# Kernel tuning notes

Hardware: AMD Instinct MI355X
Metric: run time of the kernel (lower is better)

The kernel has to match this reference:

```python
import jax, jax.numpy as jnp
import numpy as np

DIM = 1536; NH = 12; HD = 128; C2 = HD // 2          # rope half-dim = 64
F, H, W = 1, 30, 52
FRAME = H * W                                         # 1560 tokens/frame
SINK_FRAMES = 1; LOCAL_ATTN = 6
SINK = SINK_FRAMES * FRAME                            # 1560
MAX_ATTN = LOCAL_ATTN * 1560                          # 9360
CACHE = 9360                                          # kv cache length
GLOBAL_END = 9360; LOCAL_END_CACHE = 9360             # cache state before step
SPLITS = (C2 - 2 * (C2 // 3), C2 // 3, C2 // 3)       # (22, 21, 21)
EPS = 1e-6


def setup_inputs() -> dict:
    key = jax.random.key(0)
    ks = jax.random.split(key, 12)
    s = F * H * W
    rn = lambda k, sh, sc=1.0: jax.random.normal(k, sh, jnp.float32) * sc
    x = rn(ks[0], (1, s, DIM))
    Wq = rn(ks[1], (DIM, DIM), 0.02); Wk = rn(ks[2], (DIM, DIM), 0.02)
    Wv = rn(ks[3], (DIM, DIM), 0.02); Wo = rn(ks[4], (DIM, DIM), 0.02)
    zb = jnp.zeros((DIM,), jnp.float32)
    angles = jax.random.uniform(ks[5], (1024, C2), jnp.float32) * (2.0 * np.pi)
    freqs_cos = jnp.cos(angles); freqs_sin = jnp.sin(angles)
    cache_k = rn(ks[6], (1, CACHE, NH, HD)); cache_v = rn(ks[7], (1, CACHE, NH, HD))
    return dict(x=x, Wq=Wq, bq=zb, Wk=Wk, bk=zb, Wv=Wv, bv=zb, Wo=Wo, bo=zb,
                nq_w=jnp.ones((DIM,), jnp.float32), nk_w=jnp.ones((DIM,), jnp.float32),
                cache_k=cache_k, cache_v=cache_v,
                freqs_cos=freqs_cos, freqs_sin=freqs_sin,
                seq_lens=jnp.array([s], jnp.int32),
                grid_sizes=jnp.array([[F, H, W]], jnp.int32),
                current_start=GLOBAL_END)


def _rmsnorm(x, w):
    return x * jax.lax.rsqrt(jnp.mean(x * x, -1, keepdims=True) + EPS) * w


def _grid_table(table, start_frame):
    """table [1024, C2] -> per-token rope factors [S, 1, C2] over the (F,H,W) grid."""
    s0, s1, s2 = SPLITS
    tf, th, tw = table[:, :s0], table[:, s0:s0 + s1], table[:, s0 + s1:]
    fp = jnp.broadcast_to(tf[start_frame:start_frame + F][:, None, None, :], (F, H, W, s0))
    hp = jnp.broadcast_to(th[:H][None, :, None, :], (F, H, W, s1))
    wp = jnp.broadcast_to(tw[:W][None, None, :, :], (F, H, W, s2))
    return jnp.concatenate([fp, hp, wp], -1).reshape(F * H * W, 1, C2)


def _rope(x, cos, sin):
    # x: [b, s, n, d]; cos/sin: [s, 1, C2] (complex multiply in real arithmetic)
    b, s, n, d = x.shape
    xp = x.reshape(b, s, n, d // 2, 2)
    xr, xi = xp[..., 0], xp[..., 1]
    c, sn = cos[None], sin[None]                      # [1, s, 1, C2]
    out_r = xr * c - xi * sn
    out_i = xr * sn + xi * c
    return jnp.stack([out_r, out_i], -1).reshape(b, s, n, d)


def reference(x, Wq, bq, Wk, bk, Wv, bv, Wo, bo, nq_w, nk_w,
              cache_k, cache_v, freqs_cos, freqs_sin,
              seq_lens, grid_sizes, current_start):
    b, s = x.shape[:2]
    q = _rmsnorm(x @ Wq.T + bq, nq_w).reshape(b, s, NH, HD)
    k = _rmsnorm(x @ Wk.T + bk, nk_w).reshape(b, s, NH, HD)
    v = (x @ Wv.T + bv).reshape(b, s, NH, HD)

    start_frame = int(current_start) // FRAME
    cos = _grid_table(freqs_cos, start_frame)
    sin = _grid_table(freqs_sin, start_frame)
    rq = _rope(q, cos, sin)
    rk = _rope(k, cos, sin)

    # --- static cache bookkeeping (roll_and_insert path; all Python ints) ---
    num_new = s
    current_end = int(current_start) + num_new
    num_evicted = num_new + LOCAL_END_CACHE - CACHE           # 1560
    num_rolled = LOCAL_END_CACHE - num_evicted - SINK         # 6240
    local_end = LOCAL_END_CACHE + current_end - GLOBAL_END - num_evicted  # 9360
    local_start = local_end - num_new                         # 7800 == SINK + num_rolled
    temp_k = jnp.concatenate(
        [cache_k[:, :SINK], cache_k[:, SINK + num_evicted:SINK + num_evicted + num_rolled], rk], axis=1)
    temp_v = jnp.concatenate(
        [cache_v[:, :SINK], cache_v[:, SINK + num_evicted:SINK + num_evicted + num_rolled], v], axis=1)

    # --- sink + sliding-window attention ---
    local_budget = MAX_ATTN - SINK
    win_start = max(SINK, local_end - local_budget)
    k_cat = jnp.concatenate([temp_k[:, :SINK], temp_k[:, win_start:local_end]], axis=1)
    v_cat = jnp.concatenate([temp_v[:, :SINK], temp_v[:, win_start:local_end]], axis=1)

    logits = jnp.einsum('bqhd,bkhd->bhqk', rq, k_cat) * (HD ** -0.5)
    probs = jax.nn.softmax(logits, axis=-1)
    out = jnp.einsum('bhqk,bkhd->bqhd', probs, v_cat)
    y = out.reshape(b, s, DIM) @ Wo.T + bo
    return y
```

## Files before the change

kernel.cpp:

```cpp
#include <hip/hip_runtime.h>
#include <hip/hip_bf16.h>

typedef __bf16 bf16;
typedef __bf16 bf16x2 __attribute__((ext_vector_type(2)));
typedef __bf16 bf16x4 __attribute__((ext_vector_type(4)));
typedef __bf16 bf16x8 __attribute__((ext_vector_type(8)));
typedef float f32x4 __attribute__((ext_vector_type(4)));
typedef float f32x16 __attribute__((ext_vector_type(16)));

#define DIM 1536
#define NH 12
#define HD 128
#define SEQ 1560
#define KV 9360
#define KVP 9408
#define SINK 1560
#define NEWBASE 7800
#define QSCALE_L2E (0.08838834764831845f * 1.4426950408889634f)
#define NSPLIT 3
#define CHUNK 3136
#define NT 49
#define QBLK 128
#define NQT 13

__device__ __forceinline__ void gl_lds16(const void* g, void* l) {
  __builtin_amdgcn_global_load_lds(
      (const __attribute__((address_space(1))) unsigned int*)g,
      (__attribute__((address_space(3))) unsigned int*)l, 16, 0, 0);
}

__device__ __forceinline__ f32x16 mfma32(bf16x8 a, bf16x8 b, f32x16 c) {
  return __builtin_amdgcn_mfma_f32_32x32x16_bf16(a, b, c, 0, 0, 0);
}

struct CastBatch {
  const float* src[5];
  bf16* dst[5];
  int n[5];
};
__global__ __launch_bounds__(256) void castall(CastBatch cb) {
  const float* src = cb.src[blockIdx.y];
  bf16* dst = cb.dst[blockIdx.y];
  int n = cb.n[blockIdx.y];
  int i = (blockIdx.x * 256 + threadIdx.x) * 8;
  if (i < n) {
    float4 a = *(const float4*)(src + i);
    float4 b = *(const float4*)(src + i + 4);
    bf16x8 o;
    o[0] = (bf16)a.x; o[1] = (bf16)a.y; o[2] = (bf16)a.z; o[3] = (bf16)a.w;
    o[4] = (bf16)b.x; o[5] = (bf16)b.y; o[6] = (bf16)b.z; o[7] = (bf16)b.w;
    *(bf16x8*)(dst + i) = o;
  }
}

__global__ __launch_bounds__(256) void clear_pad(bf16* __restrict__ Kcat,
                                                 bf16* __restrict__ Vt) {
  int h = blockIdx.y;
  int i = blockIdx.x * 256 + threadIdx.x;
  if (i < (KVP - KV) * HD) {
    int r = KV + i / HD, d = i % HD;
    Kcat[((size_t)h * KVP + r) * HD + d] = (bf16)0.f;
    int dv = i / (KVP - KV), j = KV + i % (KVP - KV);
    Vt[((size_t)h * HD + dv) * KVP + j] = (bf16)0.f;
  }
}

struct GemmBatch {
  const bf16* B[3];
  const float* bias[3];
  float* C[3];
};

#define BM 128
#define BN 128
#define BK 32

__global__ __launch_bounds__(256, 2) void gemm_bt(const bf16* __restrict__ A,
                                                  GemmBatch gb, int M) {
  const bf16* Bw = gb.B[blockIdx.z];
  const float* bias = gb.bias[blockIdx.z];
  float* C = gb.C[blockIdx.z];
  int bm = blockIdx.x * BM;
  int bn = blockIdx.y * BN;

  __shared__ bf16 Alds[2][BM][BK];
  __shared__ bf16 Blds[2][BN][BK];

  int t = threadIdx.x;
  int lane = t & 63;
  int wave = t >> 6;
  int wr = wave >> 1, wc = wave & 1;
  int fr = lane & 15;
  int fo = (lane >> 4) * 8;

  f32x4 acc[4][4] = {};

  const int NK = DIM / BK;
  int colA = (lane & 3) * 8;
  int lrow = lane >> 2;

#define STAGEG(buf, k0)                                                     \
  {                                                                         \
    _Pragma("unroll") for (int p = 0; p < 2; ++p) {                         \
      int rbase = wave * 16 + p * 64;                                       \
      int ga = bm + rbase + lrow;                                           \
      if (ga > M - 1) ga = M - 1;                                           \
      gl_lds16(A + (size_t)ga * DIM + (k0) + colA, &Alds[buf][rbase][0]);   \
      int gbv = bn + rbase + lrow;                                          \
      gl_lds16(Bw + (size_t)gbv * DIM + (k0) + colA, &Blds[buf][rbase][0]); \
    }                                                                       \
  }

  STAGEG(0, 0);
  int cur = 0;
  for (int ks = 0; ks < NK; ++ks) {
    __syncthreads();
    if (ks + 1 < NK) STAGEG(cur ^ 1, (ks + 1) * BK);
    bf16x8 af[4], bfv[4];
#pragma unroll
    for (int i = 0; i < 4; ++i)
      af[i] = *(const bf16x8*)&Alds[cur][wr * 64 + i * 16 + fr][fo];
#pragma unroll
    for (int j = 0; j < 4; ++j)
      bfv[j] = *(const bf16x8*)&Blds[cur][wc * 64 + j * 16 + fr][fo];
#pragma unroll
    for (int i = 0; i < 4; ++i)
#pragma unroll
      for (int j = 0; j < 4; ++j)
        acc[i][j] = __builtin_amdgcn_mfma_f32_16x16x32_bf16(af[i], bfv[j],
                                                            acc[i][j], 0, 0, 0);
    cur ^= 1;
  }
#undef STAGEG

  int g4 = (lane >> 4) * 4;
#pragma unroll
  for (int i = 0; i < 4; ++i) {
    int mbase = bm + wr * 64 + i * 16 + g4;
#pragma unroll
    for (int j = 0; j < 4; ++j) {
      int col = bn + wc * 64 + j * 16 + fr;
      float bv = bias[col];
#pragma unroll
      for (int r = 0; r < 4; ++r) {
        int m = mbase + r;
        if (m < M) C[(size_t)m * DIM + col] = acc[i][j][r] + bv;
      }
    }
  }
}

__global__ __launch_bounds__(256) void norm_rope(
    const float* __restrict__ qraw, const float* __restrict__ kraw,
    const float* __restrict__ nqw, const float* __restrict__ nkw,
    const float* __restrict__ fcos, const float* __restrict__ fsin,
    bf16* __restrict__ Qh, bf16* __restrict__ Kcat) {
  int tok = blockIdx.x;
  int tid = threadIdx.x;
  const float* qr = qraw + (size_t)tok * DIM;
  const float* kr = kraw + (size_t)tok * DIM;
  float sq = 0.f, sk = 0.f;
  for (int c = tid; c < DIM; c += 256) {
    float a = qr[c];
    sq += a * a;
    float b = kr[c];
    sk += b * b;
  }
#pragma unroll
  for (int off = 32; off; off >>= 1) {
    sq += __shfl_down(sq, off);
    sk += __shfl_down(sk, off);
  }
  __shared__ float red[2][4];
  int w = tid >> 6;
  if ((tid & 63) == 0) {
    red[0][w] = sq;
    red[1][w] = sk;
  }
  __syncthreads();
  sq = red[0][0] + red[0][1] + red[0][2] + red[0][3];
  sk = red[1][0] + red[1][1] + red[1][2] + red[1][3];
  float rsq = rsqrtf(sq * (1.0f / DIM) + 1e-6f);
  float rsk = rsqrtf(sk * (1.0f / DIM) + 1e-6f);

  int hrow = tok / 52, wrow = tok % 52;
  for (int p = tid; p < NH * 64; p += 256) {
    int n = p >> 6, i = p & 63;
    int trow = (i < 22) ? 6 : (i < 43 ? hrow : wrow);
    float cs = fcos[trow * 64 + i];
    float sn = fsin[trow * 64 + i];
    int c = n * HD + 2 * i;
    float xr = qr[c] * rsq * nqw[c];
    float xi = qr[c + 1] * rsq * nqw[c + 1];
    bf16x2 qo;
    qo[0] = (bf16)((xr * cs - xi * sn) * QSCALE_L2E);
    qo[1] = (bf16)((xr * sn + xi * cs) * QSCALE_L2E);
    *(bf16x2*)(Qh + ((size_t)n * SEQ + tok) * HD + 2 * i) = qo;
    float yr = kr[c] * rsk * nkw[c];
    float yi = kr[c + 1] * rsk * nkw[c + 1];
    bf16x2 ko;
    ko[0] = (bf16)(yr * cs - yi * sn);
    ko[1] = (bf16)(yr * sn + yi * cs);
    *(bf16x2*)(Kcat + ((size_t)n * KVP + NEWBASE + tok) * HD + 2 * i) = ko;
  }
}

__global__ __launch_bounds__(256) void build_kcat(const float* __restrict__ cache_k,
                                                  bf16* __restrict__ Kcat) {
  int j = blockIdx.x;
  int src = j < SINK ? j : j + SINK;
  const float* sp = cache_k + (size_t)src * DIM;
  for (int c4 = threadIdx.x; c4 < DIM / 4; c4 += 256) {
    float4 v = *(const float4*)(sp + c4 * 4);
    int c = c4 * 4;
    int n = c >> 7, d = c & 127;
    bf16x4 o;
    o[0] = (bf16)v.x; o[1] = (bf16)v.y; o[2] = (bf16)v.z; o[3] = (bf16)v.w;
    *(bf16x4*)(Kcat + ((size_t)n * KVP + j) * HD + d) = o;
  }
}

__global__ __launch_bounds__(256) void build_vt(const float* __restrict__ cache_v,
                                                const float* __restrict__ vraw,
                                                bf16* __restrict__ Vt) {
  int h = blockIdx.y;
  int j0 = blockIdx.x * 64;
  __shared__ bf16 T[128][72];
  int tid = threadIdx.x;
  for (int idx = tid; idx < 64 * 32; idx += 256) {
    int jl = idx >> 5, s = idx & 31;
    int j = j0 + jl;
    if (j >= KV) continue;
    const float* sp;
    if (j < NEWBASE) {
      int srcj = j < SINK ? j : j + SINK;
      sp = cache_v + (size_t)srcj * DIM + h * HD;
    } else {
      sp = vraw + (size_t)(j - NEWBASE) * DIM + h * HD;
    }
    float4 v = *(const float4*)(sp + s * 4);
    T[s * 4 + 0][jl] = (bf16)v.x;
    T[s * 4 + 1][jl] = (bf16)v.y;
    T[s * 4 + 2][jl] = (bf16)v.z;
    T[s * 4 + 3][jl] = (bf16)v.w;
  }
  __syncthreads();
  for (int idx = tid; idx < 128 * 16; idx += 256) {
    int d = idx >> 4, g = idx & 15;
    int j = j0 + g * 4;
    if (j + 4 > KV) continue;
    bf16x4 o;
    o[0] = T[d][4 * g];
    o[1] = T[d][4 * g + 1];
    o[2] = T[d][4 * g + 2];
    o[3] = T[d][4 * g + 3];
    *(bf16x4*)(Vt + ((size_t)h * HD + d) * KVP + j) = o;
  }
}

__global__ __launch_bounds__(256, 2) void attn_split(const bf16* __restrict__ Qh,
                                                     const bf16* __restrict__ Kcat,
                                                     const bf16* __restrict__ Vtg,
                                                     float* __restrict__ Opart,
                                                     float* __restrict__ MLpart) {
  int orig = blockIdx.x;
  int xcd = orig & 7, jj = orig >> 3;
  int wgid = (xcd < 4 ? xcd * 59 : 236 + (xcd - 4) * 58) + jj;
  int qt = wgid % NQT;
  int h = (wgid / NQT) % NH;
  int sp = wgid / (NQT * NH);
  int q0 = qt * QBLK;
  int c0 = sp * CHUNK;

  int t = threadIdx.x, lane = t & 63, w = t >> 6;
  int ql = lane & 31, hi = lane >> 5;

  __shared__ __align__(16) bf16 Klds[2][64 * 128];
  __shared__ __align__(16) bf16 Vlds[2][128 * 64];

  int qrow = q0 + w * 32 + ql;
  int qcl = qrow < SEQ ? qrow : SEQ - 1;
  const bf16* Qp = Qh + ((size_t)h * SEQ + qcl) * HD + hi * 8;
  bf16x8 qreg[8];
#pragma unroll
  for (int ks = 0; ks < 8; ++ks) qreg[ks] = *(const bf16x8*)(Qp + ks * 16);

  int kadd[4], vadd[4];
#pragma unroll
  for (int p = 0; p < 4; ++p) {
    int rK = (4 * w + p) * 4 + (lane >> 4);
    int cK = (lane & 15) ^ (rK & 15);
    kadd[p] = rK * HD + cK * 8;
    int dV = (4 * w + p) * 8 + (lane >> 3);
    int cV = (lane & 7) ^ (dV & 7);
    vadd[p] = dV * KVP + cV * 8;
  }

  int koff[2][8];
#pragma unroll
  for (int kb = 0; kb < 2; ++kb)
#pragma unroll
    for (int ks = 0; ks < 8; ++ks)
      koff[kb][ks] = (kb * 32 + ql) * 256 + (((ks * 2 + hi) ^ (ql & 15)) * 16);
  int voff[4][4];
#pragma unroll
  for (int db = 0; db < 4; ++db)
#pragma unroll
    for (int ks = 0; ks < 4; ++ks)
      voff[db][ks] = (db * 32 + ql) * 128 + (((ks * 2 + hi) ^ (ql & 7)) * 16);

  const bf16* Khp = Kcat + (size_t)h * KVP * HD;
  const bf16* Vhp = Vtg + (size_t)h * HD * KVP;

  f32x16 oacc[4] = {};
  float m_q = -1e38f, l_q = 0.f;

#define STAGE(buf, j0)                                                        \
  {                                                                           \
    const bf16* Ks = Khp + (size_t)(j0)*HD;                                   \
    const bf16* Vs = Vhp + (j0);                                              \
    _Pragma("unroll") for (int p = 0; p < 4; ++p) {                           \
      gl_lds16(Ks + kadd[p], (char*)&Klds[buf][0] + w * 4096 + p * 1024);     \
      gl_lds16(Vs + vadd[p], (char*)&Vlds[buf][0] + w * 4096 + p * 1024);     \
    }                                                                         \
  }

  STAGE(0, c0);
  __syncthreads();
  int cur = 0;

  for (int ti = 0; ti < NT; ++ti) {
    int j0 = c0 + ti * 64;
    if (ti + 1 < NT) STAGE(cur ^ 1, j0 + 64);

    const char* Kc = (const char*)&Klds[cur][0];
    const char* Vc = (const char*)&Vlds[cur][0];

    f32x16 s0 = {}, s1 = {};
    __builtin_amdgcn_s_setprio(1);
#pragma unroll
    for (int ks = 0; ks < 8; ++ks) {
      s0 = mfma32(*(const bf16x8*)(Kc + koff[0][ks]), qreg[ks], s0);
      s1 = mfma32(*(const bf16x8*)(Kc + koff[1][ks]), qreg[ks], s1);
    }
    __builtin_amdgcn_s_setprio(0);

    if (j0 + 64 > KV) {
#pragma unroll
      for (int reg = 0; reg < 16; ++reg) {
        int kk = (reg & 3) + 8 * (reg >> 2) + 4 * hi;
        if (j0 + kk >= KV) s0[reg] = -1e38f;
        if (j0 + 32 + kk >= KV) s1[reg] = -1e38f;
      }
    }

    f32x16 mm;
#pragma unroll
    for (int r = 0; r < 16; ++r) mm[r] = fmaxf(s0[r], s1[r]);
    float m8[8];
#pragma unroll
    for (int r = 0; r < 8; ++r) m8[r] = fmaxf(mm[r], mm[r + 8]);
    float mx = fmaxf(fmaxf(fmaxf(m8[0], m8[4]), fmaxf(m8[1], m8[5])),
                     fmaxf(fmaxf(m8[2], m8[6]), fmaxf(m8[3], m8[7])));
    mx = fmaxf(mx, __shfl_xor(mx, 32));

    if (__any(mx - m_q > 8.f)) {
      float mnew = fmaxf(m_q, mx);
      float corr = exp2f(m_q - mnew);
      m_q = mnew;
      l_q *= corr;
#pragma unroll
      for (int reg = 0; reg < 16; ++reg) {
        int qsrc = (reg & 3) + 8 * (reg >> 2) + 4 * hi;
        float c = __shfl(corr, qsrc);
#pragma unroll
        for (int db = 0; db < 4; ++db) oacc[db][reg] *= c;
      }
    }

#pragma unroll
    for (int r = 0; r < 16; ++r) {
      s0[r] = exp2f(s0[r] - m_q);
      s1[r] = exp2f(s1[r] - m_q);
    }
    f32x16 ss;
#pragma unroll
    for (int r = 0; r < 16; ++r) ss[r] = s0[r] + s1[r];
    float t8[8];
#pragma unroll
    for (int r = 0; r < 8; ++r) t8[r] = ss[r] + ss[r + 8];
    float sum = ((t8[0] + t8[4]) + (t8[1] + t8[5])) +
                ((t8[2] + t8[6]) + (t8[3] + t8[7]));
    sum += __shfl_xor(sum, 32);
    l_q += sum;

    bf16x8 pa[4];
#pragma unroll
    for (int ks = 0; ks < 4; ++ks) {
      const f32x16& S = (ks < 2) ? s0 : s1;
      const int r0 = (ks & 1) * 8;
      bf16x2 p0, p1, p2, p3;
      p0[0] = (bf16)S[r0 + 0]; p0[1] = (bf16)S[r0 + 1];
      p1[0] = (bf16)S[r0 + 2]; p1[1] = (bf16)S[r0 + 3];
      p2[0] = (bf16)S[r0 + 4]; p2[1] = (bf16)S[r0 + 5];
      p3[0] = (bf16)S[r0 + 6]; p3[1] = (bf16)S[r0 + 7];
      int x0 = __builtin_bit_cast(int, p0);
      int x1 = __builtin_bit_cast(int, p1);
      int y0 = __builtin_bit_cast(int, p2);
      int y1 = __builtin_bit_cast(int, p3);
      int sx0 = __shfl_xor(x0, 32);
      int sx1 = __shfl_xor(x1, 32);
      int sy0 = __shfl_xor(y0, 32);
      int sy1 = __shfl_xor(y1, 32);
      int4 tmp;
      tmp.x = hi ? sy0 : x0;
      tmp.y = hi ? sy1 : x1;
      tmp.z = hi ? y0 : sx0;
      tmp.w = hi ? y1 : sx1;
      pa[ks] = __builtin_bit_cast(bf16x8, tmp);
    }

    __builtin_amdgcn_s_setprio(1);
#pragma unroll
    for (int db = 0; db < 4; ++db)
#pragma unroll
      for (int ks = 0; ks < 4; ++ks)
        oacc[db] = mfma32(pa[ks], *(const bf16x8*)(Vc + voff[db][ks]), oacc[db]);
    __builtin_amdgcn_s_setprio(0);

    __syncthreads();
    cur ^= 1;
  }
#undef STAGE

  float* Oh = Opart + ((size_t)sp * NH + h) * SEQ * HD;
  float* MLh = MLpart + ((size_t)sp * NH + h) * SEQ * 2;
#pragma unroll
  for (int reg = 0; reg < 16; ++reg) {
    int q = q0 + w * 32 + (reg & 3) + 8 * (reg >> 2) + 4 * hi;
    if (q >= SEQ) continue;
#pragma unroll
    for (int db = 0; db < 4; ++db)
      Oh[(size_t)q * HD + db * 32 + ql] = oacc[db][reg];
  }
  if (lane < 32) {
    int q = q0 + w * 32 + ql;
    if (q < SEQ) {
      MLh[q * 2 + 0] = m_q;
      MLh[q * 2 + 1] = l_q;
    }
  }
}

__global__ __launch_bounds__(256) void attn_merge(const float* __restrict__ Opart,
                                                  const float* __restrict__ MLpart,
                                                  bf16* __restrict__ Aout) {
  int idx = blockIdx.x * 2 + (threadIdx.x >> 7);
  if (idx >= NH * SEQ) return;
  int d = threadIdx.x & 127;
  int h = idx / SEQ, q = idx % SEQ;
  float m[NSPLIT];
  float M = -1e38f;
#pragma unroll
  for (int s = 0; s < NSPLIT; ++s) {
    m[s] = MLpart[(((size_t)s * NH + h) * SEQ + q) * 2];
    M = fmaxf(M, m[s]);
  }
  float L = 0.f, o = 0.f;
#pragma unroll
  for (int s = 0; s < NSPLIT; ++s) {
    float wgt = exp2f(m[s] - M);
    L += MLpart[(((size_t)s * NH + h) * SEQ + q) * 2 + 1] * wgt;
    o += Opart[((((size_t)s * NH + h) * SEQ + q)) * HD + d] * wgt;
  }
  Aout[(size_t)q * DIM + h * HD + d] = (bf16)(o / L);
}

extern "C" void kernel_launch(void* const* d_in, const int* in_sizes, int n_in,
                              void* d_out, int out_size, void* d_ws, size_t ws_size,
                              hipStream_t stream) {
  const float* x = (const float*)d_in[0];
  const float* Wq = (const float*)d_in[1];
  const float* bq = (const float*)d_in[2];
  const float* Wk = (const float*)d_in[3];
  const float* bk = (const float*)d_in[4];
  const float* Wv = (const float*)d_in[5];
  const float* bv = (const float*)d_in[6];
  const float* Wo = (const float*)d_in[7];
  const float* bo = (const float*)d_in[8];
  const float* nqw = (const float*)d_in[9];
  const float* nkw = (const float*)d_in[10];
  const float* cache_k = (const float*)d_in[11];
  const float* cache_v = (const float*)d_in[12];
  const float* fcos = (const float*)d_in[13];
  const float* fsin = (const float*)d_in[14];
  float* out = (float*)d_out;

  char* ws = (char*)d_ws;
  size_t off = 0;
  auto alloc = [&](size_t bytes) {
    char* p = ws + off;
    off += (bytes + 255) & ~(size_t)255;
    return p;
  };
  const int XN = SEQ * DIM;
  const int WN = DIM * DIM;
  bf16* xb = (bf16*)alloc((size_t)XN * 2);
  bf16* Wqb = (bf16*)alloc((size_t)WN * 2);
  bf16* Wkb = (bf16*)alloc((size_t)WN * 2);
  bf16* Wvb = (bf16*)alloc((size_t)WN * 2);
  bf16* Wob = (bf16*)alloc((size_t)WN * 2);
  bf16* QhB = (bf16*)alloc((size_t)NH * SEQ * HD * 2);
  bf16* Kcat = (bf16*)alloc((size_t)NH * KVP * HD * 2);
  bf16* Vt = (bf16*)alloc((size_t)NH * HD * KVP * 2);
  bf16* Aout = (bf16*)alloc((size_t)XN * 2);
  float* MLpart = (float*)alloc((size_t)NSPLIT * NH * SEQ * 2 * 4);
  float* Opart = (float*)alloc((size_t)NSPLIT * NH * SEQ * HD * 4);
  float* qraw = Opart;
  float* kraw = qraw + XN;
  float* vraw = kraw + XN;

  CastBatch cb;
  cb.src[0] = x;  cb.dst[0] = xb;  cb.n[0] = XN;
  cb.src[1] = Wq; cb.dst[1] = Wqb; cb.n[1] = WN;
  cb.src[2] = Wk; cb.dst[2] = Wkb; cb.n[2] = WN;
  cb.src[3] = Wv; cb.dst[3] = Wvb; cb.n[3] = WN;
  cb.src[4] = Wo; cb.dst[4] = Wob; cb.n[4] = WN;
  castall<<<dim3((XN + 2047) / 2048, 5), 256, 0, stream>>>(cb);

  clear_pad<<<dim3(((KVP - KV) * HD + 255) / 256, NH), 256, 0, stream>>>(Kcat, Vt);

  GemmBatch gqkv;
  gqkv.B[0] = Wqb; gqkv.B[1] = Wkb; gqkv.B[2] = Wvb;
  gqkv.bias[0] = bq; gqkv.bias[1] = bk; gqkv.bias[2] = bv;
  gqkv.C[0] = qraw; gqkv.C[1] = kraw; gqkv.C[2] = vraw;
  gemm_bt<<<dim3(13, 12, 3), 256, 0, stream>>>(xb, gqkv, SEQ);

  norm_rope<<<SEQ, 256, 0, stream>>>(qraw, kraw, nqw, nkw, fcos, fsin, QhB, Kcat);
  build_kcat<<<NEWBASE, 256, 0, stream>>>(cache_k, Kcat);
  build_vt<<<dim3(147, NH), 256, 0, stream>>>(cache_v, vraw, Vt);

  attn_split<<<dim3(NQT * NH * NSPLIT), 256, 0, stream>>>(QhB, Kcat, Vt, Opart, MLpart);
  attn_merge<<<(NH * SEQ + 1) / 2, 256, 0, stream>>>(Opart, MLpart, Aout);

  GemmBatch gout;
  gout.B[0] = Wob; gout.B[1] = Wob; gout.B[2] = Wob;
  gout.bias[0] = bo; gout.bias[1] = bo; gout.bias[2] = bo;
  gout.C[0] = out; gout.C[1] = out; gout.C[2] = out;
  gemm_bt<<<dim3(13, 12, 1), 256, 0, stream>>>(Aout, gout, SEQ);
}
```

Baseline: 310.4 us.

## Halve KV tile to 32, double split count, raise occupancy, use permlane32_swap

The attention kernel now processes 32 keys per tile instead of 64 and splits the KV range into 6 chunks instead of 3. This doubles the number of workgroups and halves LDS and register use, and launch bounds now ask for 4 waves per SIMD to hide latency better. The P-matrix lane exchange uses permlane32_swap in place of four shuffles plus selects. In exchange there are twice as many loop iterations with syncs, less MFMA work per barrier, and more partial outputs for the combine step to merge. The host launch grid and combine kernel must match the new split count, and that code is not visible here.

```diff
diff --git a/kernel.cpp b/kernel.cpp
--- a/kernel.cpp
+++ b/kernel.cpp
@@ -7,6 +7,7 @@
 typedef __bf16 bf16x8 __attribute__((ext_vector_type(8)));
 typedef float f32x4 __attribute__((ext_vector_type(4)));
 typedef float f32x16 __attribute__((ext_vector_type(16)));
+typedef unsigned u32x2 __attribute__((ext_vector_type(2)));
 
 #define DIM 1536
 #define NH 12
@@ -17,9 +18,10 @@
 #define SINK 1560
 #define NEWBASE 7800
 #define QSCALE_L2E (0.08838834764831845f * 1.4426950408889634f)
-#define NSPLIT 3
-#define CHUNK 3136
+#define NSPLIT 6
+#define CHUNK 1568
 #define NT 49
+#define KB 32
 #define QBLK 128
 #define NQT 13
 
@@ -258,25 +260,25 @@
   }
 }
 
-__global__ __launch_bounds__(256, 2) void attn_split(const bf16* __restrict__ Qh,
+__global__ __launch_bounds__(256, 4) void attn_split(const bf16* __restrict__ Qh,
                                                      const bf16* __restrict__ Kcat,
                                                      const bf16* __restrict__ Vtg,
                                                      float* __restrict__ Opart,
                                                      float* __restrict__ MLpart) {
   int orig = blockIdx.x;
-  int xcd = orig & 7, jj = orig >> 3;
-  int wgid = (xcd < 4 ? xcd * 59 : 236 + (xcd - 4) * 58) + jj;
+  int wgid = (orig & 7) * 117 + (orig >> 3);
   int qt = wgid % NQT;
-  int h = (wgid / NQT) % NH;
-  int sp = wgid / (NQT * NH);
+  int rest = wgid / NQT;
+  int h = rest % NH;
+  int sp = rest / NH;
   int q0 = qt * QBLK;
   int c0 = sp * CHUNK;
 
   int t = threadIdx.x, lane = t & 63, w = t >> 6;
   int ql = lane & 31, hi = lane >> 5;
 
-  __shared__ __align__(16) bf16 Klds[2][64 * 128];
-  __shared__ __align__(16) bf16 Vlds[2][128 * 64];
+  __shared__ __align__(16) bf16 Klds[2][KB * 128];
+  __shared__ __align__(16) bf16 Vlds[2][128 * KB];
 
   int qrow = q0 + w * 32 + ql;
   int qcl = qrow < SEQ ? qrow : SEQ - 1;
@@ -285,29 +287,26 @@
 #pragma unroll
   for (int ks = 0; ks < 8; ++ks) qreg[ks] = *(const bf16x8*)(Qp + ks * 16);
 
-  int kadd[4], vadd[4];
-#pragma unroll
-  for (int p = 0; p < 4; ++p) {
-    int rK = (4 * w + p) * 4 + (lane >> 4);
-    int cK = (lane & 15) ^ (rK & 15);
-    kadd[p] = rK * HD + cK * 8;
-    int dV = (4 * w + p) * 8 + (lane >> 3);
-    int cV = (lane & 7) ^ (dV & 7);
-    vadd[p] = dV * KVP + cV * 8;
-  }
-
-  int koff[2][8];
-#pragma unroll
-  for (int kb = 0; kb < 2; ++kb)
-#pragma unroll
-    for (int ks = 0; ks < 8; ++ks)
-      koff[kb][ks] = (kb * 32 + ql) * 256 + (((ks * 2 + hi) ^ (ql & 15)) * 16);
-  int voff[4][4];
+  int kadd[2], vadd[2];
+#pragma unroll
+  for (int p = 0; p < 2; ++p) {
+    int m = (2 * w + p) * 64 + lane;
+    int rK = m >> 4, cK = m & 15;
+    kadd[p] = rK * HD + (cK ^ (rK & 15)) * 8;
+    int dV = m >> 2, cV = m & 3;
+    vadd[p] = dV * KVP + (cV ^ (dV & 3)) * 8;
+  }
+
+  int koff[8];
+#pragma unroll
+  for (int ks = 0; ks < 8; ++ks)
+    koff[ks] = ql * 256 + (((ks * 2 + hi) ^ (ql & 15)) * 16);
+  int voff[4][2];
 #pragma unroll
   for (int db = 0; db < 4; ++db)
 #pragma unroll
-    for (int ks = 0; ks < 4; ++ks)
-      voff[db][ks] = (db * 32 + ql) * 128 + (((ks * 2 + hi) ^ (ql & 7)) * 16);
+    for (int ks = 0; ks < 2; ++ks)
+      voff[db][ks] = (db * 32 + ql) * 64 + (((ks * 2 + hi) ^ (ql & 3)) * 16);
 
   const bf16* Khp = Kcat + (size_t)h * KVP * HD;
   const bf16* Vhp = Vtg + (size_t)h * HD * KVP;
@@ -319,9 +318,9 @@
   {                                                                           \
     const bf16* Ks = Khp + (size_t)(j0)*HD;                                   \
     const bf16* Vs = Vhp + (j0);                                              \
-    _Pragma("unroll") for (int p = 0; p < 4; ++p) {                           \
-      gl_lds16(Ks + kadd[p], (char*)&Klds[buf][0] + w * 4096 + p * 1024);     \
-      gl_lds16(Vs + vadd[p], (char*)&Vlds[buf][0] + w * 4096 + p * 1024);     \
+    _Pragma("unroll") for (int p = 0; p < 2; ++p) {                           \
+      gl_lds16(Ks + kadd[p], (char*)&Klds[buf][0] + w * 2048 + p * 1024);     \
+      gl_lds16(Vs + vadd[p], (char*)&Vlds[buf][0] + w * 2048 + p * 1024);     \
     }                                                                         \
   }
 
@@ -330,36 +329,30 @@
   int cur = 0;
 
   for (int ti = 0; ti < NT; ++ti) {
-    int j0 = c0 + ti * 64;
-    if (ti + 1 < NT) STAGE(cur ^ 1, j0 + 64);
+    int j0 = c0 + ti * KB;
+    if (ti + 1 < NT) STAGE(cur ^ 1, j0 + KB);
 
     const char* Kc = (const char*)&Klds[cur][0];
     const char* Vc = (const char*)&Vlds[cur][0];
 
-    f32x16 s0 = {}, s1 = {};
+    f32x16 s0 = {};
     __builtin_amdgcn_s_setprio(1);
 #pragma unroll
-    for (int ks = 0; ks < 8; ++ks) {
-      s0 = mfma32(*(const bf16x8*)(Kc + koff[0][ks]), qreg[ks], s0);
-      s1 = mfma32(*(const bf16x8*)(Kc + koff[1][ks]), qreg[ks], s1);
-    }
+    for (int ks = 0; ks < 8; ++ks)
+      s0 = mfma32(*(const bf16x8*)(Kc + koff[ks]), qreg[ks], s0);
     __builtin_amdgcn_s_setprio(0);
 
-    if (j0 + 64 > KV) {
+    if (j0 + KB > KV) {
 #pragma unroll
       for (int reg = 0; reg < 16; ++reg) {
         int kk = (reg & 3) + 8 * (reg >> 2) + 4 * hi;
         if (j0 + kk >= KV) s0[reg] = -1e38f;
-        if (j0 + 32 + kk >= KV) s1[reg] = -1e38f;
       }
     }
 
-    f32x16 mm;
-#pragma unroll
-    for (int r = 0; r < 16; ++r) mm[r] = fmaxf(s0[r], s1[r]);
     float m8[8];
 #pragma unroll
-    for (int r = 0; r < 8; ++r) m8[r] = fmaxf(mm[r], mm[r + 8]);
+    for (int r = 0; r < 8; ++r) m8[r] = fmaxf(s0[r], s0[r + 8]);
     float mx = fmaxf(fmaxf(fmaxf(m8[0], m8[4]), fmaxf(m8[1], m8[5])),
                      fmaxf(fmaxf(m8[2], m8[6]), fmaxf(m8[3], m8[7])));
     mx = fmaxf(mx, __shfl_xor(mx, 32));
@@ -379,44 +372,35 @@
     }
 
 #pragma unroll
-    for (int r = 0; r < 16; ++r) {
-      s0[r] = exp2f(s0[r] - m_q);
-      s1[r] = exp2f(s1[r] - m_q);
-    }
-    f32x16 ss;
-#pragma unroll
-    for (int r = 0; r < 16; ++r) ss[r] = s0[r] + s1[r];
+    for (int r = 0; r < 16; ++r) s0[r] = exp2f(s0[r] - m_q);
     float t8[8];
 #pragma unroll
-    for (int r = 0; r < 8; ++r) t8[r] = ss[r] + ss[r + 8];
+    for (int r = 0; r < 8; ++r) t8[r] = s0[r] + s0[r + 8];
     float sum = ((t8[0] + t8[4]) + (t8[1] + t8[5])) +
                 ((t8[2] + t8[6]) + (t8[3] + t8[7]));
     sum += __shfl_xor(sum, 32);
     l_q += sum;
 
-    bf16x8 pa[4];
-#pragma unroll
-    for (int ks = 0; ks < 4; ++ks) {
-      const f32x16& S = (ks < 2) ? s0 : s1;
-      const int r0 = (ks & 1) * 8;
+    bf16x8 pa[2];
+#pragma unroll
+    for (int ks = 0; ks < 2; ++ks) {
+      const int r0 = ks * 8;
       bf16x2 p0, p1, p2, p3;
-      p0[0] = (bf16)S[r0 + 0]; p0[1] = (bf16)S[r0 + 1];
-      p1[0] = (bf16)S[r0 + 2]; p1[1] = (bf16)S[r0 + 3];
-      p2[0] = (bf16)S[r0 + 4]; p2[1] = (bf16)S[r0 + 5];
-      p3[0] = (bf16)S[r0 + 6]; p3[1] = (bf16)S[r0 + 7];
-      int x0 = __builtin_bit_cast(int, p0);
-      int x1 = __builtin_bit_cast(int, p1);
-      int y0 = __builtin_bit_cast(int, p2);
-      int y1 = __builtin_bit_cast(int, p3);
-      int sx0 = __shfl_xor(x0, 32);
-      int sx1 = __shfl_xor(x1, 32);
-      int sy0 = __shfl_xor(y0, 32);
-      int sy1 = __shfl_xor(y1, 32);
+      p0[0] = (bf16)s0[r0 + 0]; p0[1] = (bf16)s0[r0 + 1];
+      p1[0] = (bf16)s0[r0 + 2]; p1[1] = (bf16)s0[r0 + 3];
+      p2[0] = (bf16)s0[r0 + 4]; p2[1] = (bf16)s0[r0 + 5];
+      p3[0] = (bf16)s0[r0 + 6]; p3[1] = (bf16)s0[r0 + 7];
+      unsigned x0 = __builtin_bit_cast(unsigned, p0);
+      unsigned x1 = __builtin_bit_cast(unsigned, p1);
+      unsigned y0 = __builtin_bit_cast(unsigned, p2);
+      unsigned y1 = __builtin_bit_cast(unsigned, p3);
+      u32x2 r0v = __builtin_amdgcn_permlane32_swap(x0, y0, false, false);
+      u32x2 r1v = __builtin_amdgcn_permlane32_swap(x1, y1, false, false);
       int4 tmp;
-      tmp.x = hi ? sy0 : x0;
-      tmp.y = hi ? sy1 : x1;
-      tmp.z = hi ? y0 : sx0;
-      tmp.w = hi ? y1 : sx1;
+      tmp.x = (int)r0v[0];
+      tmp.y = (int)r1v[0];
+      tmp.z = (int)r0v[1];
+      tmp.w = (int)r1v[1];
       pa[ks] = __builtin_bit_cast(bf16x8, tmp);
     }
 
@@ -424,7 +408,7 @@
 #pragma unroll
     for (int db = 0; db < 4; ++db)
 #pragma unroll
-      for (int ks = 0; ks < 4; ++ks)
+      for (int ks = 0; ks < 2; ++ks)
         oacc[db] = mfma32(pa[ks], *(const bf16x8*)(Vc + voff[db][ks]), oacc[db]);
     __builtin_amdgcn_s_setprio(0);
 
```

Result: slower. 383.3 us (+23.5%).
